# Kernel optimization log

Measured on AMD Instinct MI355X. Metric: run time of the kernel, lower is better.

Reference implementation:

```python
import jax, jax.numpy as jnp
import numpy as np

B, T, Dx, H, K = 32, 4096, 128, 128, 10


def setup_inputs() -> dict:
    key = jax.random.key(0)
    ks = jax.random.split(key, 11)
    s = 1.0 / np.sqrt(H)  # PyTorch GRU init range

    def p(k, shape):
        return jax.random.uniform(k, shape, jnp.float32, -s, s)

    return {
        "x": jax.random.normal(ks[0], (B, T, Dx), jnp.float32),
        # forward-direction GRU params (gate order: r, z, n as in PyTorch)
        "W_ih_f": p(ks[1], (3 * H, Dx)),
        "W_hh_f": p(ks[2], (3 * H, H)),
        "b_ih_f": p(ks[3], (3 * H,)),
        "b_hh_f": p(ks[4], (3 * H,)),
        # backward-direction GRU params
        "W_ih_b": p(ks[5], (3 * H, Dx)),
        "W_hh_b": p(ks[6], (3 * H, H)),
        "b_ih_b": p(ks[7], (3 * H,)),
        "b_hh_b": p(ks[8], (3 * H,)),
        # final linear classifier
        "W_fc": p(ks[9], (K, 2 * H)),
        "b_fc": p(ks[10], (K,)),
    }


def _gru_scan(x, Wih, Whh, bih, bhh, reverse):
    """Single-direction GRU over time. x: [B,T,Dx] -> [B,T,H]."""
    # Precompute all input projections at once: [T, B, 3H]
    xp = jnp.einsum('btd,gd->tbg', x, Wih) + bih
    Whh_T = Whh.T
    Hd = Whh.shape[1]

    def cell(h, xt):
        hp = h @ Whh_T + bhh            # [B, 3H]
        xr, xz, xn = jnp.split(xt, 3, axis=-1)
        hr, hz, hn = jnp.split(hp, 3, axis=-1)
        r = jax.nn.sigmoid(xr + hr)
        z = jax.nn.sigmoid(xz + hz)
        n = jnp.tanh(xn + r * hn)
        h_new = (1.0 - z) * n + z * h
        return h_new, h_new

    h0 = jnp.zeros((x.shape[0], Hd), x.dtype)
    _, hs = jax.lax.scan(cell, h0, xp, reverse=reverse)  # [T, B, H]
    return jnp.transpose(hs, (1, 0, 2))


def reference(x, W_ih_f, W_hh_f, b_ih_f, b_hh_f,
              W_ih_b, W_hh_b, b_ih_b, b_hh_b, W_fc, b_fc):
    hf = _gru_scan(x, W_ih_f, W_hh_f, b_ih_f, b_hh_f, reverse=False)
    hb = _gru_scan(x, W_ih_b, W_hh_b, b_ih_b, b_hh_b, reverse=True)
    h = jnp.concatenate([hf, hb], axis=-1)  # [B, T, 2H]
    return h @ W_fc.T + b_fc                # [B, T, K]
```

## Files before the change

kernel.cpp:

```cpp
#include <hip/hip_runtime.h>
#include <cstdint>
#include <cstddef>

#define T_LEN   4096
#define B_SZ    32
#define H_DIM   128
#define DX      128
#define K_CLS   10
#define CHUNK   32
#define NCHUNKS (T_LEN / CHUNK)
#define XA_LD   136
#define HIST_LD 136

typedef _Float16 half2v  __attribute__((ext_vector_type(2)));
typedef _Float16 half8   __attribute__((ext_vector_type(8)));
typedef float    floatx4 __attribute__((ext_vector_type(4)));

__device__ __forceinline__ float dot2f(unsigned int w, unsigned int h, float acc) {
  return __builtin_amdgcn_fdot2(__builtin_bit_cast(half2v, w),
                                __builtin_bit_cast(half2v, h), acc, false);
}

__device__ __forceinline__ unsigned int packh2(float a, float b) {
  half2v h;
  h.x = (_Float16)a;
  h.y = (_Float16)b;
  return __builtin_bit_cast(unsigned int, h);
}

__device__ __forceinline__ float dpp_xor1_add(float x) {
  int xi = __builtin_bit_cast(int, x);
  int yi = __builtin_amdgcn_update_dpp(xi, xi, 0xB1, 0xF, 0xF, false);
  return x + __builtin_bit_cast(float, yi);
}

__device__ __forceinline__ float sigm(float x) {
  x = fminf(fmaxf(x, -30.f), 30.f);
  return __builtin_amdgcn_rcpf(1.f + __expf(-x));
}

__device__ __forceinline__ float tanhfast(float x) {
  x = fminf(fmaxf(x, -15.f), 15.f);
  float t = __expf(-2.f * x);
  return (1.f - t) * __builtin_amdgcn_rcpf(1.f + t);
}

__global__ void __launch_bounds__(256) init_out_kernel(float* __restrict__ out,
                                                       const float* __restrict__ bfc) {
  int i = blockIdx.x * 256 + threadIdx.x;
  if (i < B_SZ * T_LEN * K_CLS) out[i] = bfc[i % K_CLS];
}

__global__ void __launch_bounds__(256, 1)
gru_bidir_kernel(const float* __restrict__ x,
                 const float* __restrict__ Wih_f, const float* __restrict__ Whh_f,
                 const float* __restrict__ bih_f, const float* __restrict__ bhh_f,
                 const float* __restrict__ Wih_b, const float* __restrict__ Whh_b,
                 const float* __restrict__ bih_b, const float* __restrict__ bhh_b,
                 const float* __restrict__ Wfc, float* __restrict__ out) {
  const int tid = threadIdx.x;
  const int bid = blockIdx.x;
  const int b   = bid & (B_SZ - 1);
  const int dir = bid >> 5;

  const float* Wih = dir ? Wih_b : Wih_f;
  const float* Whh = dir ? Whh_b : Whh_f;
  const float* bih = dir ? bih_b : bih_f;
  const float* bhh = dir ? bhh_b : bhh_f;

  const int lane = tid & 63;
  const int wv   = tid >> 6;
  const int col  = lane & 15;
  const int quad = lane >> 4;
  const int j    = tid >> 1;
  const int q    = tid & 1;

  __shared__ __align__(16) _Float16 xA[CHUNK][XA_LD];
  __shared__ __align__(16) _Float16 xh2[CHUNK][4 * H_DIM];
  __shared__ __align__(16) _Float16 hist[CHUNK][HIST_LD];
  __shared__ __align__(16) _Float16 hbuf[2][H_DIM];

  unsigned int whr[32], whz[32], whn[32];
  {
    const float* Wr = Whh + (size_t)j * H_DIM + q * 64;
    const float* Wz = Whh + (size_t)(H_DIM + j) * H_DIM + q * 64;
    const float* Wn = Whh + (size_t)(2 * H_DIM + j) * H_DIM + q * 64;
#pragma unroll
    for (int i = 0; i < 32; ++i) {
      whr[i] = packh2(Wr[2 * i], Wr[2 * i + 1]);
      whz[i] = packh2(Wz[2 * i], Wz[2 * i + 1]);
      whn[i] = packh2(Wn[2 * i], Wn[2 * i + 1]);
    }
  }
  const float cbr  = bih[j] + bhh[j];
  const float cbz  = bih[H_DIM + j] + bhh[H_DIM + j];
  const float bin_ = bih[2 * H_DIM + j];
  const float bhn  = bhh[2 * H_DIM + j];

  half8 fcfrag[4];
#pragma unroll
  for (int ks = 0; ks < 4; ++ks) {
    half8 v;
#pragma unroll
    for (int e = 0; e < 8; ++e) {
      int cc = ks * 32 + quad * 8 + e;
      v[e] = (col < K_CLS) ? (_Float16)Wfc[(size_t)col * (2 * H_DIM) + dir * H_DIM + cc]
                           : (_Float16)0.f;
    }
    fcfrag[ks] = v;
  }

  if (tid < 128) hbuf[0][tid] = (_Float16)0.f;

  const int s_row = tid >> 3;
  const int cbase = (tid & 7) * 16;
  float4 px0, px1, px2, px3;
  {
    int t0 = dir ? (T_LEN - 1 - s_row) : s_row;
    const float* xp = x + ((size_t)b * T_LEN + t0) * DX + cbase;
    px0 = *(const float4*)xp;       px1 = *(const float4*)(xp + 4);
    px2 = *(const float4*)(xp + 8); px3 = *(const float4*)(xp + 12);
  }

  float hold = 0.f;
  __syncthreads();

  for (int c = 0; c < NCHUNKS; ++c) {
    {
      half8 lo, hi;
      lo[0] = (_Float16)px0.x; lo[1] = (_Float16)px0.y; lo[2] = (_Float16)px0.z; lo[3] = (_Float16)px0.w;
      lo[4] = (_Float16)px1.x; lo[5] = (_Float16)px1.y; lo[6] = (_Float16)px1.z; lo[7] = (_Float16)px1.w;
      hi[0] = (_Float16)px2.x; hi[1] = (_Float16)px2.y; hi[2] = (_Float16)px2.z; hi[3] = (_Float16)px2.w;
      hi[4] = (_Float16)px3.x; hi[5] = (_Float16)px3.y; hi[6] = (_Float16)px3.z; hi[7] = (_Float16)px3.w;
      *(half8*)&xA[s_row][cbase] = lo;
      *(half8*)&xA[s_row][cbase + 8] = hi;
    }
    __syncthreads();

#pragma unroll
    for (int nt = 0; nt < 6; ++nt) {
      const int g = (wv * 6 + nt) * 16 + col;
      const float* wsrc = Wih + (size_t)g * DX + quad * 8;
      half8 bf[4];
#pragma unroll
      for (int ks = 0; ks < 4; ++ks) {
        const float* s8 = wsrc + ks * 32;
        half8 v;
#pragma unroll
        for (int e = 0; e < 8; ++e) v[e] = (_Float16)s8[e];
        bf[ks] = v;
      }
      floatx4 a0 = (floatx4){0.f, 0.f, 0.f, 0.f};
      floatx4 a1 = (floatx4){0.f, 0.f, 0.f, 0.f};
#pragma unroll
      for (int ks = 0; ks < 4; ++ks) {
        half8 af0 = *(const half8*)&xA[col][ks * 32 + quad * 8];
        half8 af1 = *(const half8*)&xA[16 + col][ks * 32 + quad * 8];
        a0 = __builtin_amdgcn_mfma_f32_16x16x32_f16(af0, bf[ks], a0, 0, 0, 0);
        a1 = __builtin_amdgcn_mfma_f32_16x16x32_f16(af1, bf[ks], a1, 0, 0, 0);
      }
      const int jj = (g & 127) * 4 + (g >> 7);
#pragma unroll
      for (int i = 0; i < 4; ++i) {
        xh2[quad * 4 + i][jj]      = (_Float16)a0[i];
        xh2[16 + quad * 4 + i][jj] = (_Float16)a1[i];
      }
    }

    if (c + 1 < NCHUNKS) {
      int s = (c + 1) * CHUNK + s_row;
      int t0 = dir ? (T_LEN - 1 - s) : s;
      const float* xp = x + ((size_t)b * T_LEN + t0) * DX + cbase;
      px0 = *(const float4*)xp;       px1 = *(const float4*)(xp + 4);
      px2 = *(const float4*)(xp + 8); px3 = *(const float4*)(xp + 12);
    }
    __syncthreads();

    int p = 0;
#pragma unroll 2
    for (int s = 0; s < CHUNK; ++s) {
      const uint2 xv = *(const uint2*)&xh2[s][j * 4];
      const uint4* hb = (const uint4*)&hbuf[p][q * 64];
      uint4 h0 = hb[0], h1 = hb[1], h2 = hb[2], h3 = hb[3];
      uint4 h4 = hb[4], h5 = hb[5], h6 = hb[6], h7 = hb[7];
      unsigned int hh[32];
      hh[0]=h0.x;  hh[1]=h0.y;  hh[2]=h0.z;  hh[3]=h0.w;
      hh[4]=h1.x;  hh[5]=h1.y;  hh[6]=h1.z;  hh[7]=h1.w;
      hh[8]=h2.x;  hh[9]=h2.y;  hh[10]=h2.z; hh[11]=h2.w;
      hh[12]=h3.x; hh[13]=h3.y; hh[14]=h3.z; hh[15]=h3.w;
      hh[16]=h4.x; hh[17]=h4.y; hh[18]=h4.z; hh[19]=h4.w;
      hh[20]=h5.x; hh[21]=h5.y; hh[22]=h5.z; hh[23]=h5.w;
      hh[24]=h6.x; hh[25]=h6.y; hh[26]=h6.z; hh[27]=h6.w;
      hh[28]=h7.x; hh[29]=h7.y; hh[30]=h7.z; hh[31]=h7.w;

      float ar0 = 0.f, ar1 = 0.f, az0 = 0.f, az1 = 0.f, an0 = 0.f, an1 = 0.f;
#pragma unroll
      for (int i = 0; i < 16; ++i) {
        ar0 = dot2f(whr[2 * i],     hh[2 * i],     ar0);
        ar1 = dot2f(whr[2 * i + 1], hh[2 * i + 1], ar1);
        az0 = dot2f(whz[2 * i],     hh[2 * i],     az0);
        az1 = dot2f(whz[2 * i + 1], hh[2 * i + 1], az1);
        an0 = dot2f(whn[2 * i],     hh[2 * i],     an0);
        an1 = dot2f(whn[2 * i + 1], hh[2 * i + 1], an1);
      }
      float ar = dpp_xor1_add(ar0 + ar1);
      float az = dpp_xor1_add(az0 + az1);
      float an = dpp_xor1_add(an0 + an1);

      half2v x01 = __builtin_bit_cast(half2v, xv.x);
      half2v x23 = __builtin_bit_cast(half2v, xv.y);
      float rr = sigm((float)x01.x + cbr + ar);
      float zz = sigm((float)x01.y + cbz + az);
      float nn = tanhfast((float)x23.x + bin_ + rr * (an + bhn));
      hold = nn + zz * (hold - nn);

      if (q == 0) {
        _Float16 hf = (_Float16)hold;
        hbuf[p ^ 1][j] = hf;
        hist[s][j] = hf;
      }
      p ^= 1;
      __syncthreads();
    }

    if (wv < 2) {
      const int mt = wv;
      floatx4 facc = (floatx4){0.f, 0.f, 0.f, 0.f};
#pragma unroll
      for (int ks = 0; ks < 4; ++ks) {
        half8 af = *(const half8*)&hist[mt * 16 + col][ks * 32 + quad * 8];
        facc = __builtin_amdgcn_mfma_f32_16x16x32_f16(af, fcfrag[ks], facc, 0, 0, 0);
      }
      if (col < K_CLS) {
#pragma unroll
        for (int i = 0; i < 4; ++i) {
          int s = mt * 16 + quad * 4 + i;
          int t = c * CHUNK + s;
          int tt = dir ? (T_LEN - 1 - t) : t;
          atomicAdd(out + ((size_t)b * T_LEN + tt) * K_CLS + col, facc[i]);
        }
      }
    }
  }
}

extern "C" void kernel_launch(void* const* d_in, const int* in_sizes, int n_in,
                              void* d_out, int out_size, void* d_ws, size_t ws_size,
                              hipStream_t stream) {
  (void)in_sizes; (void)n_in; (void)d_ws; (void)ws_size; (void)out_size;
  const float* x     = (const float*)d_in[0];
  const float* Wih_f = (const float*)d_in[1];
  const float* Whh_f = (const float*)d_in[2];
  const float* bih_f = (const float*)d_in[3];
  const float* bhh_f = (const float*)d_in[4];
  const float* Wih_b = (const float*)d_in[5];
  const float* Whh_b = (const float*)d_in[6];
  const float* bih_b = (const float*)d_in[7];
  const float* bhh_b = (const float*)d_in[8];
  const float* Wfc   = (const float*)d_in[9];
  const float* bfc   = (const float*)d_in[10];
  float* out = (float*)d_out;

  const int n_out = B_SZ * T_LEN * K_CLS;
  init_out_kernel<<<(n_out + 255) / 256, 256, 0, stream>>>(out, bfc);
  gru_bidir_kernel<<<B_SZ * 2, 256, 0, stream>>>(x, Wih_f, Whh_f, bih_f, bhh_f,
                                                 Wih_b, Whh_b, bih_b, bhh_b, Wfc, out);
}
```

Before: 2.005 ms.

## Compute GRU recurrent matvec with MFMA across eight waves per block

Replaces the per-thread fdot2 recurrent dot products with 16x16x32 MFMA tiles. Each of eight waves owns 16 hidden units and holds the W_hh and W_ih fragments in registers. The block grows to 512 threads. The hidden state is read from a history buffer whose row 0 carries the state from the previous chunk. Input biases are folded into the fp16 input projection. Only one row of each MFMA A-tile is non-zero, so most of the matrix work is wasted, in exchange for shorter per-step VALU chains and more waves hiding latency.

```diff
diff --git a/kernel.cpp b/kernel.cpp
--- a/kernel.cpp
+++ b/kernel.cpp
@@ -10,29 +10,11 @@
 #define CHUNK   32
 #define NCHUNKS (T_LEN / CHUNK)
 #define XA_LD   136
-#define HIST_LD 136
-
-typedef _Float16 half2v  __attribute__((ext_vector_type(2)));
+#define XP_LD   408
+#define HI_LD   136
+
 typedef _Float16 half8   __attribute__((ext_vector_type(8)));
 typedef float    floatx4 __attribute__((ext_vector_type(4)));
-
-__device__ __forceinline__ float dot2f(unsigned int w, unsigned int h, float acc) {
-  return __builtin_amdgcn_fdot2(__builtin_bit_cast(half2v, w),
-                                __builtin_bit_cast(half2v, h), acc, false);
-}
-
-__device__ __forceinline__ unsigned int packh2(float a, float b) {
-  half2v h;
-  h.x = (_Float16)a;
-  h.y = (_Float16)b;
-  return __builtin_bit_cast(unsigned int, h);
-}
-
-__device__ __forceinline__ float dpp_xor1_add(float x) {
-  int xi = __builtin_bit_cast(int, x);
-  int yi = __builtin_amdgcn_update_dpp(xi, xi, 0xB1, 0xF, 0xF, false);
-  return x + __builtin_bit_cast(float, yi);
-}
 
 __device__ __forceinline__ float sigm(float x) {
   x = fminf(fmaxf(x, -30.f), 30.f);
@@ -51,7 +33,7 @@
   if (i < B_SZ * T_LEN * K_CLS) out[i] = bfc[i % K_CLS];
 }
 
-__global__ void __launch_bounds__(256, 1)
+__global__ void __launch_bounds__(512, 2)
 gru_bidir_kernel(const float* __restrict__ x,
                  const float* __restrict__ Wih_f, const float* __restrict__ Whh_f,
                  const float* __restrict__ bih_f, const float* __restrict__ bhh_f,
@@ -72,175 +54,165 @@
   const int wv   = tid >> 6;
   const int col  = lane & 15;
   const int quad = lane >> 4;
-  const int j    = tid >> 1;
-  const int q    = tid & 1;
+  const int jloc = wv * 16 + col;
 
   __shared__ __align__(16) _Float16 xA[CHUNK][XA_LD];
-  __shared__ __align__(16) _Float16 xh2[CHUNK][4 * H_DIM];
-  __shared__ __align__(16) _Float16 hist[CHUNK][HIST_LD];
-  __shared__ __align__(16) _Float16 hbuf[2][H_DIM];
-
-  unsigned int whr[32], whz[32], whn[32];
-  {
-    const float* Wr = Whh + (size_t)j * H_DIM + q * 64;
-    const float* Wz = Whh + (size_t)(H_DIM + j) * H_DIM + q * 64;
-    const float* Wn = Whh + (size_t)(2 * H_DIM + j) * H_DIM + q * 64;
-#pragma unroll
-    for (int i = 0; i < 32; ++i) {
-      whr[i] = packh2(Wr[2 * i], Wr[2 * i + 1]);
-      whz[i] = packh2(Wz[2 * i], Wz[2 * i + 1]);
-      whn[i] = packh2(Wn[2 * i], Wn[2 * i + 1]);
-    }
-  }
-  const float cbr  = bih[j] + bhh[j];
-  const float cbz  = bih[H_DIM + j] + bhh[H_DIM + j];
-  const float bin_ = bih[2 * H_DIM + j];
-  const float bhn  = bhh[2 * H_DIM + j];
-
-  half8 fcfrag[4];
-#pragma unroll
-  for (int ks = 0; ks < 4; ++ks) {
-    half8 v;
-#pragma unroll
-    for (int e = 0; e < 8; ++e) {
-      int cc = ks * 32 + quad * 8 + e;
-      v[e] = (col < K_CLS) ? (_Float16)Wfc[(size_t)col * (2 * H_DIM) + dir * H_DIM + cc]
-                           : (_Float16)0.f;
-    }
-    fcfrag[ks] = v;
-  }
-
-  if (tid < 128) hbuf[0][tid] = (_Float16)0.f;
-
-  const int s_row = tid >> 3;
-  const int cbase = (tid & 7) * 16;
-  float4 px0, px1, px2, px3;
+  __shared__ __align__(16) _Float16 xPL[CHUNK][XP_LD];
+  __shared__ __align__(16) _Float16 hist[CHUNK + 1][HI_LD];
+
+  half8 whf[3][4];
+  half8 wif[3][4];
+#pragma unroll
+  for (int g = 0; g < 3; ++g) {
+#pragma unroll
+    for (int kt = 0; kt < 4; ++kt) {
+      const float* sh = Whh + (size_t)(g * H_DIM + jloc) * H_DIM + kt * 32 + quad * 8;
+      const float* si = Wih + (size_t)(g * H_DIM + jloc) * DX + kt * 32 + quad * 8;
+      half8 vh, vi;
+#pragma unroll
+      for (int e = 0; e < 8; ++e) {
+        vh[e] = (_Float16)sh[e];
+        vi[e] = (_Float16)si[e];
+      }
+      whf[g][kt] = vh;
+      wif[g][kt] = vi;
+    }
+  }
+  const float bias_r = bih[jloc] + bhh[jloc];
+  const float bias_z = bih[H_DIM + jloc] + bhh[H_DIM + jloc];
+  const float bias_n = bih[2 * H_DIM + jloc];
+  const float bhn    = bhh[2 * H_DIM + jloc];
+
+  half8 fcf[4];
+  if (wv < 2) {
+#pragma unroll
+    for (int kt = 0; kt < 4; ++kt) {
+      half8 v;
+#pragma unroll
+      for (int e = 0; e < 8; ++e) {
+        int k = kt * 32 + quad * 8 + e;
+        v[e] = (col < K_CLS) ? (_Float16)Wfc[(size_t)col * (2 * H_DIM) + dir * H_DIM + k]
+                             : (_Float16)0.f;
+      }
+      fcf[kt] = v;
+    }
+  }
+
+  half8 hz;
+#pragma unroll
+  for (int e = 0; e < 8; ++e) hz[e] = (_Float16)0.f;
+  half8 haf0 = hz, haf1 = hz, haf2 = hz, haf3 = hz;
+
+  if (tid < H_DIM) hist[0][tid] = (_Float16)0.f;
+
+  const int s_row = tid >> 4;
+  const int cb    = (tid & 15) * 8;
+  float4 px0, px1;
   {
     int t0 = dir ? (T_LEN - 1 - s_row) : s_row;
-    const float* xp = x + ((size_t)b * T_LEN + t0) * DX + cbase;
-    px0 = *(const float4*)xp;       px1 = *(const float4*)(xp + 4);
-    px2 = *(const float4*)(xp + 8); px3 = *(const float4*)(xp + 12);
+    const float* xr = x + ((size_t)b * T_LEN + t0) * DX + cb;
+    px0 = *(const float4*)xr;
+    px1 = *(const float4*)(xr + 4);
   }
 
   float hold = 0.f;
+  const floatx4 z4 = {0.f, 0.f, 0.f, 0.f};
   __syncthreads();
 
   for (int c = 0; c < NCHUNKS; ++c) {
     {
-      half8 lo, hi;
-      lo[0] = (_Float16)px0.x; lo[1] = (_Float16)px0.y; lo[2] = (_Float16)px0.z; lo[3] = (_Float16)px0.w;
-      lo[4] = (_Float16)px1.x; lo[5] = (_Float16)px1.y; lo[6] = (_Float16)px1.z; lo[7] = (_Float16)px1.w;
-      hi[0] = (_Float16)px2.x; hi[1] = (_Float16)px2.y; hi[2] = (_Float16)px2.z; hi[3] = (_Float16)px2.w;
-      hi[4] = (_Float16)px3.x; hi[5] = (_Float16)px3.y; hi[6] = (_Float16)px3.z; hi[7] = (_Float16)px3.w;
-      *(half8*)&xA[s_row][cbase] = lo;
-      *(half8*)&xA[s_row][cbase + 8] = hi;
+      half8 v;
+      v[0] = (_Float16)px0.x; v[1] = (_Float16)px0.y; v[2] = (_Float16)px0.z; v[3] = (_Float16)px0.w;
+      v[4] = (_Float16)px1.x; v[5] = (_Float16)px1.y; v[6] = (_Float16)px1.z; v[7] = (_Float16)px1.w;
+      *(half8*)&xA[s_row][cb] = v;
     }
     __syncthreads();
 
 #pragma unroll
-    for (int nt = 0; nt < 6; ++nt) {
-      const int g = (wv * 6 + nt) * 16 + col;
-      const float* wsrc = Wih + (size_t)g * DX + quad * 8;
-      half8 bf[4];
-#pragma unroll
-      for (int ks = 0; ks < 4; ++ks) {
-        const float* s8 = wsrc + ks * 32;
-        half8 v;
-#pragma unroll
-        for (int e = 0; e < 8; ++e) v[e] = (_Float16)s8[e];
-        bf[ks] = v;
-      }
-      floatx4 a0 = (floatx4){0.f, 0.f, 0.f, 0.f};
-      floatx4 a1 = (floatx4){0.f, 0.f, 0.f, 0.f};
-#pragma unroll
-      for (int ks = 0; ks < 4; ++ks) {
-        half8 af0 = *(const half8*)&xA[col][ks * 32 + quad * 8];
-        half8 af1 = *(const half8*)&xA[16 + col][ks * 32 + quad * 8];
-        a0 = __builtin_amdgcn_mfma_f32_16x16x32_f16(af0, bf[ks], a0, 0, 0, 0);
-        a1 = __builtin_amdgcn_mfma_f32_16x16x32_f16(af1, bf[ks], a1, 0, 0, 0);
-      }
-      const int jj = (g & 127) * 4 + (g >> 7);
-#pragma unroll
-      for (int i = 0; i < 4; ++i) {
-        xh2[quad * 4 + i][jj]      = (_Float16)a0[i];
-        xh2[16 + quad * 4 + i][jj] = (_Float16)a1[i];
+    for (int mt = 0; mt < 2; ++mt) {
+      half8 af[4];
+#pragma unroll
+      for (int kt = 0; kt < 4; ++kt)
+        af[kt] = *(const half8*)&xA[mt * 16 + col][kt * 32 + quad * 8];
+#pragma unroll
+      for (int g = 0; g < 3; ++g) {
+        floatx4 a = z4;
+#pragma unroll
+        for (int kt = 0; kt < 4; ++kt)
+          a = __builtin_amdgcn_mfma_f32_16x16x32_f16(af[kt], wif[g][kt], a, 0, 0, 0);
+        float bb = (g == 0) ? bias_r : (g == 1) ? bias_z : bias_n;
+#pragma unroll
+        for (int i = 0; i < 4; ++i)
+          xPL[mt * 16 + quad * 4 + i][g * H_DIM + jloc] = (_Float16)(a[i] + bb);
       }
     }
 
     if (c + 1 < NCHUNKS) {
-      int s = (c + 1) * CHUNK + s_row;
+      int s  = (c + 1) * CHUNK + s_row;
       int t0 = dir ? (T_LEN - 1 - s) : s;
-      const float* xp = x + ((size_t)b * T_LEN + t0) * DX + cbase;
-      px0 = *(const float4*)xp;       px1 = *(const float4*)(xp + 4);
-      px2 = *(const float4*)(xp + 8); px3 = *(const float4*)(xp + 12);
+      const float* xr = x + ((size_t)b * T_LEN + t0) * DX + cb;
+      px0 = *(const float4*)xr;
+      px1 = *(const float4*)(xr + 4);
     }
     __syncthreads();
 
-    int p = 0;
 #pragma unroll 2
     for (int s = 0; s < CHUNK; ++s) {
-      const uint2 xv = *(const uint2*)&xh2[s][j * 4];
-      const uint4* hb = (const uint4*)&hbuf[p][q * 64];
-      uint4 h0 = hb[0], h1 = hb[1], h2 = hb[2], h3 = hb[3];
-      uint4 h4 = hb[4], h5 = hb[5], h6 = hb[6], h7 = hb[7];
-      unsigned int hh[32];
-      hh[0]=h0.x;  hh[1]=h0.y;  hh[2]=h0.z;  hh[3]=h0.w;
-      hh[4]=h1.x;  hh[5]=h1.y;  hh[6]=h1.z;  hh[7]=h1.w;
-      hh[8]=h2.x;  hh[9]=h2.y;  hh[10]=h2.z; hh[11]=h2.w;
-      hh[12]=h3.x; hh[13]=h3.y; hh[14]=h3.z; hh[15]=h3.w;
-      hh[16]=h4.x; hh[17]=h4.y; hh[18]=h4.z; hh[19]=h4.w;
-      hh[20]=h5.x; hh[21]=h5.y; hh[22]=h5.z; hh[23]=h5.w;
-      hh[24]=h6.x; hh[25]=h6.y; hh[26]=h6.z; hh[27]=h6.w;
-      hh[28]=h7.x; hh[29]=h7.y; hh[30]=h7.z; hh[31]=h7.w;
-
-      float ar0 = 0.f, ar1 = 0.f, az0 = 0.f, az1 = 0.f, an0 = 0.f, an1 = 0.f;
-#pragma unroll
-      for (int i = 0; i < 16; ++i) {
-        ar0 = dot2f(whr[2 * i],     hh[2 * i],     ar0);
-        ar1 = dot2f(whr[2 * i + 1], hh[2 * i + 1], ar1);
-        az0 = dot2f(whz[2 * i],     hh[2 * i],     az0);
-        az1 = dot2f(whz[2 * i + 1], hh[2 * i + 1], az1);
-        an0 = dot2f(whn[2 * i],     hh[2 * i],     an0);
-        an1 = dot2f(whn[2 * i + 1], hh[2 * i + 1], an1);
-      }
-      float ar = dpp_xor1_add(ar0 + ar1);
-      float az = dpp_xor1_add(az0 + az1);
-      float an = dpp_xor1_add(an0 + an1);
-
-      half2v x01 = __builtin_bit_cast(half2v, xv.x);
-      half2v x23 = __builtin_bit_cast(half2v, xv.y);
-      float rr = sigm((float)x01.x + cbr + ar);
-      float zz = sigm((float)x01.y + cbz + az);
-      float nn = tanhfast((float)x23.x + bin_ + rr * (an + bhn));
+      if (col == 0) {
+        haf0 = *(const half8*)&hist[s][quad * 8];
+        haf1 = *(const half8*)&hist[s][32 + quad * 8];
+        haf2 = *(const half8*)&hist[s][64 + quad * 8];
+        haf3 = *(const half8*)&hist[s][96 + quad * 8];
+      }
+      floatx4 arA = __builtin_amdgcn_mfma_f32_16x16x32_f16(haf0, whf[0][0], z4, 0, 0, 0);
+      arA = __builtin_amdgcn_mfma_f32_16x16x32_f16(haf1, whf[0][1], arA, 0, 0, 0);
+      floatx4 arB = __builtin_amdgcn_mfma_f32_16x16x32_f16(haf2, whf[0][2], z4, 0, 0, 0);
+      arB = __builtin_amdgcn_mfma_f32_16x16x32_f16(haf3, whf[0][3], arB, 0, 0, 0);
+
+      floatx4 azA = __builtin_amdgcn_mfma_f32_16x16x32_f16(haf0, whf[1][0], z4, 0, 0, 0);
+      azA = __builtin_amdgcn_mfma_f32_16x16x32_f16(haf1, whf[1][1], azA, 0, 0, 0);
+      floatx4 azB = __builtin_amdgcn_mfma_f32_16x16x32_f16(haf2, whf[1][2], z4, 0, 0, 0);
+      azB = __builtin_amdgcn_mfma_f32_16x16x32_f16(haf3, whf[1][3], azB, 0, 0, 0);
+
+      floatx4 anA = __builtin_amdgcn_mfma_f32_16x16x32_f16(haf0, whf[2][0], z4, 0, 0, 0);
+      anA = __builtin_amdgcn_mfma_f32_16x16x32_f16(haf1, whf[2][1], anA, 0, 0, 0);
+      floatx4 anB = __builtin_amdgcn_mfma_f32_16x16x32_f16(haf2, whf[2][2], z4, 0, 0, 0);
+      anB = __builtin_amdgcn_mfma_f32_16x16x32_f16(haf3, whf[2][3], anB, 0, 0, 0);
+
+      float ar = arA[0] + arB[0];
+      float az = azA[0] + azB[0];
+      float an = anA[0] + anB[0];
+
+      float xr = (float)xPL[s][jloc];
+      float xz = (float)xPL[s][H_DIM + jloc];
+      float xn = (float)xPL[s][2 * H_DIM + jloc];
+
+      float rr = sigm(xr + ar);
+      float zz = sigm(xz + az);
+      float nn = tanhfast(xn + rr * (an + bhn));
       hold = nn + zz * (hold - nn);
 
-      if (q == 0) {
-        _Float16 hf = (_Float16)hold;
-        hbuf[p ^ 1][j] = hf;
-        hist[s][j] = hf;
-      }
-      p ^= 1;
+      if (quad == 0) hist[s + 1][jloc] = (_Float16)hold;
       __syncthreads();
     }
 
     if (wv < 2) {
-      const int mt = wv;
-      floatx4 facc = (floatx4){0.f, 0.f, 0.f, 0.f};
-#pragma unroll
-      for (int ks = 0; ks < 4; ++ks) {
-        half8 af = *(const half8*)&hist[mt * 16 + col][ks * 32 + quad * 8];
-        facc = __builtin_amdgcn_mfma_f32_16x16x32_f16(af, fcfrag[ks], facc, 0, 0, 0);
+      floatx4 fa = z4;
+#pragma unroll
+      for (int kt = 0; kt < 4; ++kt) {
+        half8 af = *(const half8*)&hist[1 + wv * 16 + col][kt * 32 + quad * 8];
+        fa = __builtin_amdgcn_mfma_f32_16x16x32_f16(af, fcf[kt], fa, 0, 0, 0);
       }
       if (col < K_CLS) {
 #pragma unroll
         for (int i = 0; i < 4; ++i) {
-          int s = mt * 16 + quad * 4 + i;
-          int t = c * CHUNK + s;
+          int t  = c * CHUNK + wv * 16 + quad * 4 + i;
           int tt = dir ? (T_LEN - 1 - t) : t;
-          atomicAdd(out + ((size_t)b * T_LEN + tt) * K_CLS + col, facc[i]);
+          atomicAdd(out + ((size_t)b * T_LEN + tt) * K_CLS + col, fa[i]);
         }
       }
     }
+    if (tid >= 256 && tid < 256 + H_DIM) hist[0][tid - 256] = hist[CHUNK][tid - 256];
   }
 }
 
@@ -263,6 +235,6 @@
 
   const int n_out = B_SZ * T_LEN * K_CLS;
   init_out_kernel<<<(n_out + 255) / 256, 256, 0, stream>>>(out, bfc);
-  gru_bidir_kernel<<<B_SZ * 2, 256, 0, stream>>>(x, Wih_f, Whh_f, bih_f, bhh_f,
+  gru_bidir_kernel<<<B_SZ * 2, 512, 0, stream>>>(x, Wih_f, Whh_f, bih_f, bhh_f,
                                                  Wih_b, Whh_b, bih_b, bhh_b, Wfc, out);
 }
```

New measurement: 1.810 ms. -9.7%, faster.
